# Performance work log

Hardware: AMD Instinct MI355X
Metric: run time of the kernel (lower is better)

Reference implementation:

```python
import jax, jax.numpy as jnp
import numpy as np

K = 4          # kNN neighbors (includes self, distance 0)
NUM_CONVS = 3


def _mlp(h, Ws, bs):
    # Linear -> ELU repeated, final Linear has no activation (matches nn.Sequential)
    for i, (W, b) in enumerate(zip(Ws, bs)):
        h = h @ W + b
        if i < len(Ws) - 1:
            h = jax.nn.elu(h)
    return h


def _gravnet(emb, Ws, bs, Wh, bh, Wo1, Wo2, bo2):
    # PyG GravNetConv: project to learned space s and features h, kNN in s,
    # edge weight exp(-10*d^2), mean+max aggregate, out = lin_out1(x) + lin_out2(agg)
    s = emb @ Ws + bs                        # [B,N,S]
    h = emb @ Wh + bh                        # [B,N,P]
    sq = jnp.sum(s * s, axis=-1)             # [B,N]
    d2 = sq[:, :, None] + sq[:, None, :] - 2.0 * jnp.einsum('bns,bms->bnm', s, s)
    negd2, idx = jax.lax.top_k(-d2, K)       # [B,N,K] nearest (incl. self)
    w = jnp.exp(-10.0 * jnp.maximum(-negd2, 0.0))   # clamp tiny negative d2 from numerics
    neigh = jax.vmap(lambda hb, ib: hb[ib])(h, idx)  # [B,N,K,P]
    msg = neigh * w[..., None]
    agg = jnp.concatenate([msg.mean(axis=2), msg.max(axis=2)], axis=-1)  # [B,N,2P]
    return emb @ Wo1 + agg @ Wo2 + bo2


def setup_inputs() -> dict:
    key = jax.random.key(0)
    keys = iter(jax.random.split(key, 128))

    def lin(kin, kout, bias=True):
        lim = 1.0 / np.sqrt(kin)
        W = jax.random.uniform(next(keys), (kin, kout), minval=-lim, maxval=lim, dtype=jnp.float32)
        if not bias:
            return W
        b = jax.random.uniform(next(keys), (kout,), minval=-lim, maxval=lim, dtype=jnp.float32)
        return W, b

    d = {"x": jax.random.normal(next(keys), (8, 4096, 12), dtype=jnp.float32)}
    for name, dims in [("nn1", [12, 126, 126, 126, 32]),
                       ("nn2", [44, 256, 256, 256, 6]),
                       ("nn3", [18, 256, 256, 256, 6])]:
        for i in range(4):
            W, b = lin(dims[i], dims[i + 1])
            d[f"{name}_w{i}"] = W
            d[f"{name}_b{i}"] = b
    E, S, P = 32, 4, 8
    ws, bss, wh, bhs, wo1, wo2, bo2 = [], [], [], [], [], [], []
    for _ in range(NUM_CONVS):
        W, b = lin(E, S); ws.append(W); bss.append(b)
        W, b = lin(E, P); wh.append(W); bhs.append(b)
        wo1.append(lin(E, E, bias=False))
        W, b = lin(2 * P, E); wo2.append(W); bo2.append(b)
    d["conv_ws"] = jnp.stack(ws);  d["conv_bs"] = jnp.stack(bss)
    d["conv_wh"] = jnp.stack(wh);  d["conv_bh"] = jnp.stack(bhs)
    d["conv_wo1"] = jnp.stack(wo1)
    d["conv_wo2"] = jnp.stack(wo2); d["conv_bo2"] = jnp.stack(bo2)
    return d


def reference(x,
              nn1_w0, nn1_b0, nn1_w1, nn1_b1, nn1_w2, nn1_b2, nn1_w3, nn1_b3,
              nn2_w0, nn2_b0, nn2_w1, nn2_b1, nn2_w2, nn2_b2, nn2_w3, nn2_b3,
              nn3_w0, nn3_b0, nn3_w1, nn3_b1, nn3_w2, nn3_b2, nn3_w3, nn3_b3,
              conv_ws, conv_bs, conv_wh, conv_bh, conv_wo1, conv_wo2, conv_bo2):
    emb = _mlp(x, [nn1_w0, nn1_w1, nn1_w2, nn1_w3], [nn1_b0, nn1_b1, nn1_b2, nn1_b3])
    for i in range(NUM_CONVS):
        emb = _gravnet(emb, conv_ws[i], conv_bs[i], conv_wh[i], conv_bh[i],
                       conv_wo1[i], conv_wo2[i], conv_bo2[i])
    preds_id = _mlp(jnp.concatenate([x, emb], axis=-1),
                    [nn2_w0, nn2_w1, nn2_w2, nn2_w3], [nn2_b0, nn2_b1, nn2_b2, nn2_b3])
    preds_p4 = _mlp(jnp.concatenate([x, preds_id], axis=-1),
                    [nn3_w0, nn3_w1, nn3_w2, nn3_w3], [nn3_b0, nn3_b1, nn3_b2, nn3_b3])
    return jnp.concatenate([preds_id, preds_p4], axis=-1)  # [B,N,12]
```

## Files before the change

### kernel.cpp

```cpp
#include <hip/hip_runtime.h>
#include <hip/hip_bf16.h>
#include <cfloat>
#include <climits>

#define NN_TOTAL 32768
#define NPTS     4096

typedef __attribute__((ext_vector_type(8))) short short8;
typedef __attribute__((ext_vector_type(4))) float f32x4;

__device__ __forceinline__ void split_bf16(float v, unsigned short& h, unsigned short& l)
{
    __hip_bfloat16 hb = __float2bfloat16(v);
    float hf = __bfloat162float(hb);
    __hip_bfloat16 lb = __float2bfloat16(v - hf);
    h = __builtin_bit_cast(unsigned short, hb);
    l = __builtin_bit_cast(unsigned short, lb);
}

__device__ __forceinline__ float elu_fast(float v)
{
    return (v > 0.f) ? v : (__expf(v) - 1.f);
}

__device__ __forceinline__ void gload16(const unsigned short* g, unsigned short* l)
{
    __builtin_amdgcn_global_load_lds(
        (const __attribute__((address_space(1))) unsigned int*)g,
        (__attribute__((address_space(3))) unsigned int*)l, 16, 0, 0);
}

struct PrepArgs {
    const float* W[12];
    int K[12];
    int N[12];
    int ksh[12];
    int off[12];
    int blk0[12];
};

__global__ __launch_bounds__(256) void prep_all(
    PrepArgs a, unsigned short* __restrict__ th, unsigned short* __restrict__ tl)
{
    int l = 0;
    #pragma unroll
    for (int j = 1; j < 12; ++j) l += (blockIdx.x >= (unsigned)a.blk0[j]) ? 1 : 0;
    const int le = (blockIdx.x - a.blk0[l]) * 256 + threadIdx.x;
    const int ksh = a.ksh[l];
    const int n = le >> ksh;
    const int k = le & ((1 << ksh) - 1);
    const float v = (n < a.N[l] && k < a.K[l]) ? a.W[l][(size_t)k * a.N[l] + n] : 0.f;
    unsigned short h, lo;
    split_bf16(v, h, lo);
    th[a.off[l] + le] = h;
    tl[a.off[l] + le] = lo;
}

__global__ __launch_bounds__(256) void pack_x64(
    const float* __restrict__ x, unsigned short* __restrict__ Xh, unsigned short* __restrict__ Xl)
{
    const int gid = blockIdx.x * 256 + threadIdx.x;
    const int r = gid >> 3, c8 = (gid & 7) * 8;
    unsigned short h[8], l[8];
    #pragma unroll
    for (int j = 0; j < 8; ++j) {
        const int col = c8 + j;
        const float v = (col < 12) ? x[(size_t)r * 12 + col] : 0.f;
        split_bf16(v, h[j], l[j]);
    }
    *(int4*)(Xh + (size_t)r * 64 + c8) = *(int4*)h;
    *(int4*)(Xl + (size_t)r * 64 + c8) = *(int4*)l;
}

__global__ __launch_bounds__(256) void cat2_pack(
    const float* __restrict__ x, const float* __restrict__ emb,
    unsigned short* __restrict__ Xh, unsigned short* __restrict__ Xl)
{
    const int gid = blockIdx.x * 256 + threadIdx.x;
    const int r = gid >> 3, c8 = (gid & 7) * 8;
    unsigned short h[8], l[8];
    #pragma unroll
    for (int j = 0; j < 8; ++j) {
        const int col = c8 + j;
        float v = 0.f;
        if (col < 12)      v = x[(size_t)r * 12 + col];
        else if (col < 44) v = emb[(size_t)r * 32 + (col - 12)];
        split_bf16(v, h[j], l[j]);
    }
    *(int4*)(Xh + (size_t)r * 64 + c8) = *(int4*)h;
    *(int4*)(Xl + (size_t)r * 64 + c8) = *(int4*)l;
}

__global__ __launch_bounds__(256) void cat3_pack(
    const float* __restrict__ x, const float* __restrict__ dout,
    unsigned short* __restrict__ Xh, unsigned short* __restrict__ Xl)
{
    const int gid = blockIdx.x * 256 + threadIdx.x;
    const int r = gid >> 3, c8 = (gid & 7) * 8;
    unsigned short h[8], l[8];
    #pragma unroll
    for (int j = 0; j < 8; ++j) {
        const int col = c8 + j;
        float v = 0.f;
        if (col < 12)      v = x[(size_t)r * 12 + col];
        else if (col < 18) v = dout[(size_t)r * 12 + (col - 12)];
        split_bf16(v, h[j], l[j]);
    }
    *(int4*)(Xh + (size_t)r * 64 + c8) = *(int4*)h;
    *(int4*)(Xl + (size_t)r * 64 + c8) = *(int4*)l;
}

template<int MF, int NF>
__global__ __launch_bounds__(256, (MF == 2 ? 3 : 2)) void gemm_mfma3(
    const unsigned short* __restrict__ Ah, const unsigned short* __restrict__ Al,
    const unsigned short* __restrict__ Bh, const unsigned short* __restrict__ Bl,
    const float* __restrict__ bias, int Kp, int N, int act,
    float* __restrict__ Cf, int ldcf,
    unsigned short* __restrict__ Ch, unsigned short* __restrict__ Cl, int ldcb, int padN)
{
    constexpr int BM = MF * 32;
    __shared__ unsigned short ldsbuf[2 * BM * 64 + 2 * NF * 32 * 64];
    unsigned short* ldsAh = ldsbuf;
    unsigned short* ldsAl = ldsbuf + BM * 64;
    unsigned short* ldsBh = ldsbuf + 2 * BM * 64;
    unsigned short* ldsBl = ldsbuf + 2 * BM * 64 + NF * 32 * 64;

    const int tid  = threadIdx.x;
    const int wave = tid >> 6, lane = tid & 63;
    const int wr = wave >> 1, wc = wave & 1;
    const int row0 = blockIdx.x * BM;
    const int col0 = blockIdx.y * (NF * 32);
    const int r16 = lane & 15, kg = lane >> 4;

    f32x4 acc[MF][NF];
    #pragma unroll
    for (int m = 0; m < MF; ++m)
        #pragma unroll
        for (int n = 0; n < NF; ++n)
            #pragma unroll
            for (int r = 0; r < 4; ++r) acc[m][n][r] = 0.f;

    for (int k0 = 0; k0 < Kp; k0 += 64) {
        __syncthreads();
        #pragma unroll
        for (int c = tid; c < BM * 8; c += 256) {
            const int r  = c >> 3;
            const int kc = ((c & 7) ^ (r & 7)) * 8;
            const size_t go = (size_t)(row0 + r) * Kp + k0 + kc;
            gload16(Ah + go, ldsAh + c * 8);
            gload16(Al + go, ldsAl + c * 8);
        }
        #pragma unroll
        for (int c = tid; c < NF * 256; c += 256) {
            const int r  = c >> 3;
            const int kc = ((c & 7) ^ (r & 7)) * 8;
            const size_t go = (size_t)(col0 + r) * Kp + k0 + kc;
            gload16(Bh + go, ldsBh + c * 8);
            gload16(Bl + go, ldsBl + c * 8);
        }
        __syncthreads();

        #pragma unroll
        for (int kk = 0; kk < 2; ++kk) {
            const int lc = kk * 4 + kg;
            short8 ah[MF], al[MF], bh[NF], bl[NF];
            #pragma unroll
            for (int m = 0; m < MF; ++m) {
                const int rr = wr * (MF * 16) + m * 16 + r16;
                const int off = rr * 64 + ((lc ^ (rr & 7)) * 8);
                ah[m] = *(const short8*)&ldsAh[off];
                al[m] = *(const short8*)&ldsAl[off];
            }
            #pragma unroll
            for (int n = 0; n < NF; ++n) {
                const int br = (NF == 4 ? wc * 64 + n * 16 : wc * 16) + r16;
                const int off = br * 64 + ((lc ^ (br & 7)) * 8);
                bh[n] = *(const short8*)&ldsBh[off];
                bl[n] = *(const short8*)&ldsBl[off];
            }
            #pragma unroll
            for (int m = 0; m < MF; ++m)
                #pragma unroll
                for (int n = 0; n < NF; ++n) {
                    acc[m][n] = __builtin_amdgcn_mfma_f32_16x16x32_bf16(ah[m], bh[n], acc[m][n], 0, 0, 0);
                    acc[m][n] = __builtin_amdgcn_mfma_f32_16x16x32_bf16(ah[m], bl[n], acc[m][n], 0, 0, 0);
                    acc[m][n] = __builtin_amdgcn_mfma_f32_16x16x32_bf16(al[m], bh[n], acc[m][n], 0, 0, 0);
                }
        }
    }

    #pragma unroll
    for (int m = 0; m < MF; ++m) {
        #pragma unroll
        for (int n = 0; n < NF; ++n) {
            const int col = col0 + (NF == 4 ? wc * 64 + n * 16 : wc * 16) + r16;
            #pragma unroll
            for (int r = 0; r < 4; ++r) {
                const int row = row0 + wr * (MF * 16) + m * 16 + kg * 4 + r;
                if (col < N) {
                    float v = acc[m][n][r] + bias[col];
                    if (act) v = elu_fast(v);
                    if (Cf) {
                        Cf[(size_t)row * ldcf + col] = v;
                    } else {
                        unsigned short h, l;
                        split_bf16(v, h, l);
                        Ch[(size_t)row * ldcb + col] = h;
                        Cl[(size_t)row * ldcb + col] = l;
                    }
                } else if (Ch && col < padN) {
                    Ch[(size_t)row * ldcb + col] = 0;
                    Cl[(size_t)row * ldcb + col] = 0;
                }
            }
        }
    }
}

__global__ __launch_bounds__(64) void conv_proj(
    const float* __restrict__ emb, const float* __restrict__ Ws,
    const float* __restrict__ bs, const float* __restrict__ Wh,
    const float* __restrict__ bh,
    float* __restrict__ s_out, float* __restrict__ sq_out, float* __restrict__ h_out)
{
    __shared__ float ws_s[32 * 4];
    __shared__ float wh_s[32 * 8];
    __shared__ float bs_s[4];
    __shared__ float bh_s[8];
    const int tid = threadIdx.x;
    for (int i = tid; i < 128; i += 64) ws_s[i] = Ws[i];
    for (int i = tid; i < 256; i += 64) wh_s[i] = Wh[i];
    if (tid < 4) bs_s[tid] = bs[tid];
    if (tid >= 8 && tid < 16) bh_s[tid - 8] = bh[tid - 8];
    __syncthreads();

    const int row = blockIdx.x * 64 + tid;
    float e[32];
    #pragma unroll
    for (int i = 0; i < 8; i++)
        *(float4*)&e[i * 4] = *(const float4*)(emb + (size_t)row * 32 + i * 4);

    float sv[4];
    #pragma unroll
    for (int c = 0; c < 4; c++) {
        float a = e[0] * ws_s[c];
        #pragma unroll
        for (int k = 1; k < 32; k++) a = fmaf(e[k], ws_s[k * 4 + c], a);
        sv[c] = a + bs_s[c];
    }
    float sq = sv[0] * sv[0];
    sq = fmaf(sv[1], sv[1], sq);
    sq = fmaf(sv[2], sv[2], sq);
    sq = fmaf(sv[3], sv[3], sq);

    float hv[8];
    #pragma unroll
    for (int c = 0; c < 8; c++) {
        float a = e[0] * wh_s[c];
        #pragma unroll
        for (int k = 1; k < 32; k++) a = fmaf(e[k], wh_s[k * 8 + c], a);
        hv[c] = a + bh_s[c];
    }

    *(float4*)(s_out + (size_t)row * 4) = *(float4*)&sv[0];
    sq_out[row] = sq;
    *(float4*)(h_out + (size_t)row * 8)     = *(float4*)&hv[0];
    *(float4*)(h_out + (size_t)row * 8 + 4) = *(float4*)&hv[4];
}

__device__ __forceinline__ void merge44(const float* ad, const int* ai,
                                        const float* bd, const int* bi,
                                        float* od, int* oi)
{
    int a = 0, b = 0;
    #pragma unroll
    for (int k = 0; k < 4; ++k) {
        bool ta;
        if (a < 4 && b < 4)
            ta = (ad[a] < bd[b]) || (ad[a] == bd[b] && ai[a] < bi[b]);
        else
            ta = (a < 4);
        if (ta) { od[k] = ad[a]; oi[k] = ai[a]; ++a; }
        else    { od[k] = bd[b]; oi[k] = bi[b]; ++b; }
    }
}

__global__ __launch_bounds__(256) void knn_top4_part(
    const float* __restrict__ s, const float* __restrict__ sq,
    float* __restrict__ pd, int* __restrict__ pi)
{
    __shared__ float4 cs[256];
    __shared__ float  csq[256];

    const int tid  = threadIdx.x;
    const int pg   = blockIdx.x >> 4;
    const int sp   = blockIdx.x & 15;
    const int p0   = pg << 8;
    const int base = (p0 >> 12) << 12;
    const int row  = p0 + tid;

    const float4 sn  = *(const float4*)(s + (size_t)row * 4);
    const float  sqn = sq[row];

    const int m0 = sp << 8;
    {
        const int gm = base + m0 + tid;
        cs[tid]  = *(const float4*)(s + (size_t)gm * 4);
        csq[tid] = sq[gm];
    }
    __syncthreads();

    float bd[4] = {FLT_MAX, FLT_MAX, FLT_MAX, FLT_MAX};
    int   bi[4] = {INT_MAX, INT_MAX, INT_MAX, INT_MAX};

    #pragma unroll 8
    for (int i = 0; i < 256; ++i) {
        const float4 cm = cs[i];
        const float  cq = csq[i];
        float dot = sn.x * cm.x;
        dot = fmaf(sn.y, cm.y, dot);
        dot = fmaf(sn.z, cm.z, dot);
        dot = fmaf(sn.w, cm.w, dot);
        const float d2 = (sqn + cq) - 2.f * dot;
        const int m = m0 + i;
        const bool c3 = d2 < bd[3];
        const bool c2 = d2 < bd[2];
        const bool c1 = d2 < bd[1];
        const bool c0 = d2 < bd[0];
        bi[3] = c3 ? (c2 ? bi[2] : m) : bi[3];
        bi[2] = c2 ? (c1 ? bi[1] : m) : bi[2];
        bi[1] = c1 ? (c0 ? bi[0] : m) : bi[1];
        bi[0] = c0 ? m : bi[0];
        bd[3] = __builtin_amdgcn_fmed3f(bd[2], bd[3], d2);
        bd[2] = __builtin_amdgcn_fmed3f(bd[1], bd[2], d2);
        bd[1] = __builtin_amdgcn_fmed3f(bd[0], bd[1], d2);
        bd[0] = fminf(bd[0], d2);
    }

    const size_t o = (((size_t)pg * 16 + sp) * 256 + tid) * 4;
    *(float4*)(pd + o) = *(float4*)&bd[0];
    *(int4*)(pi + o)   = *(int4*)&bi[0];
}

__global__ __launch_bounds__(64) void conv_agg(
    const float* __restrict__ emb, const float* __restrict__ h,
    const float* __restrict__ pd, const int* __restrict__ pi,
    const float* __restrict__ Wo1, const float* __restrict__ Wo2,
    const float* __restrict__ bo2, float* __restrict__ out,
    const float* __restrict__ Ws2, const float* __restrict__ bs2,
    const float* __restrict__ Wh2, const float* __restrict__ bh2,
    float* __restrict__ s_out, float* __restrict__ sq_out, float* __restrict__ h_out)
{
    __shared__ float w1[1024];
    __shared__ float w2[512];
    __shared__ float b2[32];
    __shared__ float ws_s[128];
    __shared__ float wh_s[256];
    __shared__ float bs_s[4];
    __shared__ float bh_s[8];
    const int tid = threadIdx.x;
    for (int i = tid; i < 1024; i += 64) w1[i] = Wo1[i];
    for (int i = tid; i < 512;  i += 64) w2[i] = Wo2[i];
    if (tid < 32) b2[tid] = bo2[tid];
    if (Ws2) {
        for (int i = tid; i < 128; i += 64) ws_s[i] = Ws2[i];
        for (int i = tid; i < 256; i += 64) wh_s[i] = Wh2[i];
        if (tid < 4) bs_s[tid] = bs2[tid];
        if (tid >= 8 && tid < 16) bh_s[tid - 8] = bh2[tid - 8];
    }
    __syncthreads();

    const int row  = blockIdx.x * 64 + tid;
    const int pg   = row >> 8;
    const int ln   = row & 255;
    const int base = (row >> 12) << 12;

    float ad[4];
    int   ai[4];
    {
        const size_t o = ((size_t)pg * 16 * 256 + ln) * 4;
        *(float4*)&ad[0] = *(const float4*)(pd + o);
        *(int4*)&ai[0]   = *(const int4*)(pi + o);
    }
    #pragma unroll
    for (int sp = 1; sp < 16; ++sp) {
        const size_t o = (((size_t)pg * 16 + sp) * 256 + ln) * 4;
        float bdv[4], od[4];
        int   biv[4], oi[4];
        *(float4*)&bdv[0] = *(const float4*)(pd + o);
        *(int4*)&biv[0]   = *(const int4*)(pi + o);
        merge44(ad, ai, bdv, biv, od, oi);
        #pragma unroll
        for (int k = 0; k < 4; ++k) { ad[k] = od[k]; ai[k] = oi[k]; }
    }

    float e[32];
    #pragma unroll
    for (int i = 0; i < 8; i++)
        *(float4*)&e[i * 4] = *(const float4*)(emb + (size_t)row * 32 + i * 4);

    float msum[8], mmax[8];
    #pragma unroll
    for (int dd = 0; dd < 8; dd++) { msum[dd] = 0.f; mmax[dd] = -FLT_MAX; }

    #pragma unroll
    for (int k = 0; k < 4; k++) {
        const int g    = base + ai[k];
        const float wk = __expf(-10.f * fmaxf(ad[k], 0.f));
        float hv[8];
        *(float4*)&hv[0] = *(const float4*)(h + (size_t)g * 8);
        *(float4*)&hv[4] = *(const float4*)(h + (size_t)g * 8 + 4);
        #pragma unroll
        for (int dd = 0; dd < 8; dd++) {
            const float m = hv[dd] * wk;
            msum[dd] += m;
            mmax[dd] = fmaxf(mmax[dd], m);
        }
    }

    float agg[16];
    #pragma unroll
    for (int dd = 0; dd < 8; dd++) { agg[dd] = msum[dd] * 0.25f; agg[8 + dd] = mmax[dd]; }

    float o32[32];
    #pragma unroll
    for (int j = 0; j < 32; j++) {
        float a = e[0] * w1[j];
        #pragma unroll
        for (int k = 1; k < 32; k++) a = fmaf(e[k], w1[k * 32 + j], a);
        float g = agg[0] * w2[j];
        #pragma unroll
        for (int k = 1; k < 16; k++) g = fmaf(agg[k], w2[k * 32 + j], g);
        o32[j] = a + g + b2[j];
        out[(size_t)row * 32 + j] = o32[j];
    }

    if (Ws2) {
        float sv[4];
        #pragma unroll
        for (int c = 0; c < 4; c++) {
            float a = o32[0] * ws_s[c];
            #pragma unroll
            for (int k = 1; k < 32; k++) a = fmaf(o32[k], ws_s[k * 4 + c], a);
            sv[c] = a + bs_s[c];
        }
        float sq2 = sv[0] * sv[0];
        sq2 = fmaf(sv[1], sv[1], sq2);
        sq2 = fmaf(sv[2], sv[2], sq2);
        sq2 = fmaf(sv[3], sv[3], sq2);

        float hv[8];
        #pragma unroll
        for (int c = 0; c < 8; c++) {
            float a = o32[0] * wh_s[c];
            #pragma unroll
            for (int k = 1; k < 32; k++) a = fmaf(o32[k], wh_s[k * 8 + c], a);
            hv[c] = a + bh_s[c];
        }
        *(float4*)(s_out + (size_t)row * 4) = *(float4*)&sv[0];
        sq_out[row] = sq2;
        *(float4*)(h_out + (size_t)row * 8)     = *(float4*)&hv[0];
        *(float4*)(h_out + (size_t)row * 8 + 4) = *(float4*)&hv[4];
    }
}

extern "C" void kernel_launch(void* const* d_in, const int* in_sizes, int n_in,
                              void* d_out, int out_size, void* d_ws, size_t ws_size,
                              hipStream_t stream)
{
    const float* x = (const float*)d_in[0];
    const float* nn1_w[4] = {(const float*)d_in[1], (const float*)d_in[3], (const float*)d_in[5], (const float*)d_in[7]};
    const float* nn1_b[4] = {(const float*)d_in[2], (const float*)d_in[4], (const float*)d_in[6], (const float*)d_in[8]};
    const float* nn2_w[4] = {(const float*)d_in[9],  (const float*)d_in[11], (const float*)d_in[13], (const float*)d_in[15]};
    const float* nn2_b[4] = {(const float*)d_in[10], (const float*)d_in[12], (const float*)d_in[14], (const float*)d_in[16]};
    const float* nn3_w[4] = {(const float*)d_in[17], (const float*)d_in[19], (const float*)d_in[21], (const float*)d_in[23]};
    const float* nn3_b[4] = {(const float*)d_in[18], (const float*)d_in[20], (const float*)d_in[22], (const float*)d_in[24]};
    const float* conv_ws  = (const float*)d_in[25];
    const float* conv_bs  = (const float*)d_in[26];
    const float* conv_wh  = (const float*)d_in[27];
    const float* conv_bh  = (const float*)d_in[28];
    const float* conv_wo1 = (const float*)d_in[29];
    const float* conv_wo2 = (const float*)d_in[30];
    const float* conv_bo2 = (const float*)d_in[31];

    float* outp = (float*)d_out;
    const int M = NN_TOTAL;

    char* p = (char*)d_ws;
    auto take = [&](size_t bytes) { char* r = p; p += (bytes + 255) & ~size_t(255); return r; };
    unsigned short* Xa_h = (unsigned short*)take((size_t)M * 256 * 2);
    unsigned short* Xa_l = (unsigned short*)take((size_t)M * 256 * 2);
    unsigned short* Xb_h = (unsigned short*)take((size_t)M * 256 * 2);
    unsigned short* Xb_l = (unsigned short*)take((size_t)M * 256 * 2);
    float* embA = (float*)take((size_t)M * 32 * 4);
    float* embB = (float*)take((size_t)M * 32 * 4);
    unsigned short* WH = (unsigned short*)take((size_t)450000 * 2);
    unsigned short* WL = (unsigned short*)take((size_t)450000 * 2);

    char* q = (char*)Xa_h;
    auto takeq = [&](size_t bytes) { char* r = q; q += (bytes + 255) & ~size_t(255); return r; };
    float* sbuf  = (float*)takeq((size_t)M * 4 * 4);
    float* sqb   = (float*)takeq((size_t)M * 4);
    float* hbufA = (float*)takeq((size_t)M * 8 * 4);
    float* hbufB = (float*)takeq((size_t)M * 8 * 4);
    float* pdb   = (float*)takeq((size_t)M * 16 * 4 * 4);
    int*   pib   = (int*)takeq((size_t)M * 16 * 4 * 4);

    struct LW { int K, N, Kp, Np, off; };
    LW lw[12];
    const float* Ws_[12] = {nn1_w[0], nn1_w[1], nn1_w[2], nn1_w[3],
                            nn2_w[0], nn2_w[1], nn2_w[2], nn2_w[3],
                            nn3_w[0], nn3_w[1], nn3_w[2], nn3_w[3]};
    const int Ks_[12] = {12, 126, 126, 126,  44, 256, 256, 256,  18, 256, 256, 256};
    const int Ns_[12] = {126, 126, 126, 32,  256, 256, 256, 6,   256, 256, 256, 6};
    PrepArgs pa;
    int off = 0, blk = 0;
    for (int i = 0; i < 12; ++i) {
        lw[i].K = Ks_[i]; lw[i].N = Ns_[i];
        lw[i].Kp = (Ks_[i] + 63) & ~63;
        lw[i].Np = (Ns_[i] <= 32) ? 32 : ((Ns_[i] + 127) & ~127);
        lw[i].off = off;
        pa.W[i] = Ws_[i];
        pa.K[i] = Ks_[i]; pa.N[i] = Ns_[i];
        pa.ksh[i] = __builtin_ctz(lw[i].Kp);
        pa.off[i] = off;
        pa.blk0[i] = blk;
        off += lw[i].Kp * lw[i].Np;
        blk += lw[i].Kp * lw[i].Np / 256;
    }
    prep_all<<<blk, 256, 0, stream>>>(pa, WH, WL);

    auto mfma = [&](const unsigned short* Ah, const unsigned short* Al, int li,
                    const float* bias, int act,
                    float* Cf, int ldcf,
                    unsigned short* Chh, unsigned short* Cll, int ldcb, int padN, int nf) {
        if (nf == 4) {
            dim3 g(M / 64, lw[li].Np / 128);
            gemm_mfma3<2, 4><<<g, 256, 0, stream>>>(Ah, Al, WH + lw[li].off, WL + lw[li].off,
                                                    bias, lw[li].Kp, lw[li].N, act,
                                                    Cf, ldcf, Chh, Cll, ldcb, padN);
        } else {
            dim3 g(M / 128, 1);
            gemm_mfma3<4, 1><<<g, 256, 0, stream>>>(Ah, Al, WH + lw[li].off, WL + lw[li].off,
                                                    bias, lw[li].Kp, lw[li].N, act,
                                                    Cf, ldcf, Chh, Cll, ldcb, padN);
        }
    };

    pack_x64<<<M * 8 / 256, 256, 0, stream>>>(x, Xa_h, Xa_l);
    mfma(Xa_h, Xa_l, 0, nn1_b[0], 1, nullptr, 0, Xb_h, Xb_l, 128, 128, 4);
    mfma(Xb_h, Xb_l, 1, nn1_b[1], 1, nullptr, 0, Xa_h, Xa_l, 128, 128, 4);
    mfma(Xa_h, Xa_l, 2, nn1_b[2], 1, nullptr, 0, Xb_h, Xb_l, 128, 128, 4);
    mfma(Xb_h, Xb_l, 3, nn1_b[3], 0, embA, 32, nullptr, nullptr, 0, 0, 1);

    conv_proj<<<M / 64, 64, 0, stream>>>(
        embA, conv_ws, conv_bs, conv_wh, conv_bh, sbuf, sqb, hbufA);
    float* ecur = embA;  float* enext = embB;
    float* hcur = hbufA; float* hnext = hbufB;
    for (int i = 0; i < 3; i++) {
        knn_top4_part<<<(M / 256) * 16, 256, 0, stream>>>(sbuf, sqb, pdb, pib);
        const bool fuse = (i < 2);
        conv_agg<<<M / 64, 64, 0, stream>>>(
            ecur, hcur, pdb, pib,
            conv_wo1 + i * 1024, conv_wo2 + i * 512, conv_bo2 + i * 32, enext,
            fuse ? conv_ws + (i + 1) * 128 : nullptr,
            fuse ? conv_bs + (i + 1) * 4   : nullptr,
            fuse ? conv_wh + (i + 1) * 256 : nullptr,
            fuse ? conv_bh + (i + 1) * 8   : nullptr,
            sbuf, sqb, hnext);
        float* t = ecur; ecur = enext; enext = t;
        t = hcur; hcur = hnext; hnext = t;
    }

    cat2_pack<<<M * 8 / 256, 256, 0, stream>>>(x, ecur, Xa_h, Xa_l);
    mfma(Xa_h, Xa_l, 4, nn2_b[0], 1, nullptr, 0, Xb_h, Xb_l, 256, 256, 4);
    mfma(Xb_h, Xb_l, 5, nn2_b[1], 1, nullptr, 0, Xa_h, Xa_l, 256, 256, 4);
    mfma(Xa_h, Xa_l, 6, nn2_b[2], 1, nullptr, 0, Xb_h, Xb_l, 256, 256, 4);
    mfma(Xb_h, Xb_l, 7, nn2_b[3], 0, outp, 12, nullptr, nullptr, 0, 0, 1);

    cat3_pack<<<M * 8 / 256, 256, 0, stream>>>(x, outp, Xa_h, Xa_l);
    mfma(Xa_h, Xa_l, 8, nn3_b[0], 1, nullptr, 0, Xb_h, Xb_l, 256, 256, 4);
    mfma(Xb_h, Xb_l, 9, nn3_b[1], 1, nullptr, 0, Xa_h, Xa_l, 256, 256, 4);
    mfma(Xa_h, Xa_l, 10, nn3_b[2], 1, nullptr, 0, Xb_h, Xb_l, 256, 256, 4);
    mfma(Xb_h, Xb_l, 11, nn3_b[3], 0, outp + 6, 12, nullptr, nullptr, 0, 0, 1);
}
```

Measured before the change: 571.7 us.

## Double-buffer GEMM LDS tiles with 32-wide K steps to overlap loads and MFMA

The split-bf16 MFMA GEMM now keeps two LDS buffers and shrinks the K step from 64 to 32. The next K tile's global-to-LDS loads are issued before the current tile's MFMAs, and the block synchronises only once per step instead of twice. The aim is to hide global load latency behind matrix math; the minimum-blocks hint for the MF!=2 variant also rises from 2 to 4. The costs are twice as many loop iterations, a 4-way instead of 8-way XOR swizzle (possible LDS bank conflicts), and register pressure from the higher occupancy hint.

```diff
diff --git a/kernel.cpp b/kernel.cpp
--- a/kernel.cpp
+++ b/kernel.cpp
@@ -111,7 +111,7 @@
 }
 
 template<int MF, int NF>
-__global__ __launch_bounds__(256, (MF == 2 ? 3 : 2)) void gemm_mfma3(
+__global__ __launch_bounds__(256, (MF == 2 ? 3 : 4)) void gemm_mfma3(
     const unsigned short* __restrict__ Ah, const unsigned short* __restrict__ Al,
     const unsigned short* __restrict__ Bh, const unsigned short* __restrict__ Bl,
     const float* __restrict__ bias, int Kp, int N, int act,
@@ -119,11 +119,10 @@
     unsigned short* __restrict__ Ch, unsigned short* __restrict__ Cl, int ldcb, int padN)
 {
     constexpr int BM = MF * 32;
-    __shared__ unsigned short ldsbuf[2 * BM * 64 + 2 * NF * 32 * 64];
-    unsigned short* ldsAh = ldsbuf;
-    unsigned short* ldsAl = ldsbuf + BM * 64;
-    unsigned short* ldsBh = ldsbuf + 2 * BM * 64;
-    unsigned short* ldsBl = ldsbuf + 2 * BM * 64 + NF * 32 * 64;
+    constexpr int PA = BM * 32;
+    constexpr int PB = NF * 32 * 32;
+    constexpr int PH = 2 * PA + 2 * PB;
+    __shared__ unsigned short lds[2 * PH];
 
     const int tid  = threadIdx.x;
     const int wave = tid >> 6, lane = tid & 63;
@@ -140,53 +139,62 @@
             #pragma unroll
             for (int r = 0; r < 4; ++r) acc[m][n][r] = 0.f;
 
-    for (int k0 = 0; k0 < Kp; k0 += 64) {
-        __syncthreads();
-        #pragma unroll
-        for (int c = tid; c < BM * 8; c += 256) {
-            const int r  = c >> 3;
-            const int kc = ((c & 7) ^ (r & 7)) * 8;
+    auto STAGE = [&](int p, int k0) {
+        unsigned short* base = lds + p * PH;
+        #pragma unroll
+        for (int c = tid; c < BM * 4; c += 256) {
+            const int r  = c >> 2;
+            const int kc = ((c & 3) ^ (r & 3)) * 8;
             const size_t go = (size_t)(row0 + r) * Kp + k0 + kc;
-            gload16(Ah + go, ldsAh + c * 8);
-            gload16(Al + go, ldsAl + c * 8);
-        }
-        #pragma unroll
-        for (int c = tid; c < NF * 256; c += 256) {
-            const int r  = c >> 3;
-            const int kc = ((c & 7) ^ (r & 7)) * 8;
+            gload16(Ah + go, base + c * 8);
+            gload16(Al + go, base + PA + c * 8);
+        }
+        #pragma unroll
+        for (int c = tid; c < NF * 128; c += 256) {
+            const int r  = c >> 2;
+            const int kc = ((c & 3) ^ (r & 3)) * 8;
             const size_t go = (size_t)(col0 + r) * Kp + k0 + kc;
-            gload16(Bh + go, ldsBh + c * 8);
-            gload16(Bl + go, ldsBl + c * 8);
-        }
-        __syncthreads();
-
-        #pragma unroll
-        for (int kk = 0; kk < 2; ++kk) {
-            const int lc = kk * 4 + kg;
-            short8 ah[MF], al[MF], bh[NF], bl[NF];
-            #pragma unroll
-            for (int m = 0; m < MF; ++m) {
-                const int rr = wr * (MF * 16) + m * 16 + r16;
-                const int off = rr * 64 + ((lc ^ (rr & 7)) * 8);
-                ah[m] = *(const short8*)&ldsAh[off];
-                al[m] = *(const short8*)&ldsAl[off];
-            }
+            gload16(Bh + go, base + 2 * PA + c * 8);
+            gload16(Bl + go, base + 2 * PA + PB + c * 8);
+        }
+    };
+
+    auto COMPUTE = [&](int p) {
+        unsigned short* base = lds + p * PH;
+        short8 ah[MF], al[MF], bh[NF], bl[NF];
+        #pragma unroll
+        for (int m = 0; m < MF; ++m) {
+            const int rr = wr * (MF * 16) + m * 16 + r16;
+            const int off = rr * 32 + ((kg ^ (rr & 3)) * 8);
+            ah[m] = *(const short8*)&base[off];
+            al[m] = *(const short8*)&base[PA + off];
+        }
+        #pragma unroll
+        for (int n = 0; n < NF; ++n) {
+            const int br = (NF == 4 ? wc * 64 + n * 16 : wc * 16) + r16;
+            const int off = br * 32 + ((kg ^ (br & 3)) * 8);
+            bh[n] = *(const short8*)&base[2 * PA + off];
+            bl[n] = *(const short8*)&base[2 * PA + PB + off];
+        }
+        #pragma unroll
+        for (int m = 0; m < MF; ++m)
             #pragma unroll
             for (int n = 0; n < NF; ++n) {
-                const int br = (NF == 4 ? wc * 64 + n * 16 : wc * 16) + r16;
-                const int off = br * 64 + ((lc ^ (br & 7)) * 8);
-                bh[n] = *(const short8*)&ldsBh[off];
-                bl[n] = *(const short8*)&ldsBl[off];
+                acc[m][n] = __builtin_amdgcn_mfma_f32_16x16x32_bf16(ah[m], bh[n], acc[m][n], 0, 0, 0);
+                acc[m][n] = __builtin_amdgcn_mfma_f32_16x16x32_bf16(ah[m], bl[n], acc[m][n], 0, 0, 0);
+                acc[m][n] = __builtin_amdgcn_mfma_f32_16x16x32_bf16(al[m], bh[n], acc[m][n], 0, 0, 0);
             }
-            #pragma unroll
-            for (int m = 0; m < MF; ++m)
-                #pragma unroll
-                for (int n = 0; n < NF; ++n) {
-                    acc[m][n] = __builtin_amdgcn_mfma_f32_16x16x32_bf16(ah[m], bh[n], acc[m][n], 0, 0, 0);
-                    acc[m][n] = __builtin_amdgcn_mfma_f32_16x16x32_bf16(ah[m], bl[n], acc[m][n], 0, 0, 0);
-                    acc[m][n] = __builtin_amdgcn_mfma_f32_16x16x32_bf16(al[m], bh[n], acc[m][n], 0, 0, 0);
-                }
-        }
+    };
+
+    const int nt = Kp >> 5;
+    STAGE(0, 0);
+    __syncthreads();
+    int cur = 0;
+    for (int t = 0; t < nt; ++t) {
+        if (t + 1 < nt) STAGE(cur ^ 1, (t + 1) * 32);
+        COMPUTE(cur);
+        __syncthreads();
+        cur ^= 1;
     }
 
     #pragma unroll
```

Measured after the change: 570.9 us. No clear change (-0.1%).
